# Performance work log

Hardware: AMD Instinct MI355X
Metric: run time of the kernel (lower is better)

The kernel has to match this reference:

```python
import jax, jax.numpy as jnp
import numpy as np

N_NODES = 50000
N_EDGES = 800000
D_IN = 128
D_OUT = 128
N_GRAPHS = 64
NEG_SLOPE = 0.01  # torch F.leaky_relu default


def gcn_conv(x, W, b, src, dst, n_nodes):
    """PyG GCNConv: linear, add self-loops, symmetric norm, scatter-add, bias."""
    h = x @ W  # [N, D_OUT]
    # degree including self-loop (edge_weight = 1)
    deg = jnp.zeros((n_nodes,), x.dtype).at[dst].add(1.0) + 1.0
    dinv = jax.lax.rsqrt(deg)
    norm = dinv[src] * dinv[dst]           # [E]
    agg = jnp.zeros_like(h).at[dst].add(h[src] * norm[:, None])
    # self-loop contribution: dinv[i]*dinv[i]*h[i] = h[i]/deg[i]
    return agg + h * (1.0 / deg)[:, None] + b


def gcn_branch(x, edge_index, Ws, bs):
    src, dst = edge_index[0], edge_index[1]
    n = x.shape[0]
    for W, b in zip(Ws, bs):
        x = gcn_conv(x, W, b, src, dst, n)
        x = jax.nn.leaky_relu(x, NEG_SLOPE)
        # dropout is identity in eval mode
    return x


def mean_pool(x, batch, num_graphs):
    s = jax.ops.segment_sum(x, batch, num_segments=num_graphs)
    cnt = jax.ops.segment_sum(jnp.ones((x.shape[0],), x.dtype), batch, num_segments=num_graphs)
    return s / jnp.maximum(cnt, 1.0)[:, None]


def setup_inputs() -> dict:
    key = jax.random.key(0)
    ks = jax.random.split(key, 20)
    inp = {
        'x1': jax.random.normal(ks[0], (N_NODES, D_IN), jnp.float32),
        'edge_index1': jax.random.randint(ks[1], (2, N_EDGES), 0, N_NODES, jnp.int64 if jax.config.jax_enable_x64 else jnp.int32),
        'batch1': jnp.sort(jax.random.randint(ks[2], (N_NODES,), 0, N_GRAPHS)),
        'x2': jax.random.normal(ks[3], (N_NODES, D_IN), jnp.float32),
        'edge_index2': jax.random.randint(ks[4], (2, N_EDGES), 0, N_NODES, jnp.int64 if jax.config.jax_enable_x64 else jnp.int32),
        'batch2': jnp.sort(jax.random.randint(ks[5], (N_NODES,), 0, N_GRAPHS)),
    }
    s = 1.0 / np.sqrt(D_IN)
    inp['W1_0'] = jax.random.uniform(ks[6], (D_IN, D_OUT), jnp.float32, -s, s)
    inp['b1_0'] = jnp.zeros((D_OUT,), jnp.float32)
    inp['W1_1'] = jax.random.uniform(ks[7], (D_OUT, D_OUT), jnp.float32, -s, s)
    inp['b1_1'] = jnp.zeros((D_OUT,), jnp.float32)
    inp['W2_0'] = jax.random.uniform(ks[8], (D_IN, D_OUT), jnp.float32, -s, s)
    inp['b2_0'] = jnp.zeros((D_OUT,), jnp.float32)
    inp['W2_1'] = jax.random.uniform(ks[9], (D_OUT, D_OUT), jnp.float32, -s, s)
    inp['b2_1'] = jnp.zeros((D_OUT,), jnp.float32)
    s2 = 1.0 / np.sqrt(2 * D_OUT)
    inp['lin1_W'] = jax.random.uniform(ks[10], (2 * D_OUT, D_OUT), jnp.float32, -s2, s2)
    inp['lin1_b'] = jax.random.uniform(ks[11], (D_OUT,), jnp.float32, -s2, s2)
    s3 = 1.0 / np.sqrt(D_OUT)
    inp['lin2_W'] = jax.random.uniform(ks[12], (D_OUT, 1), jnp.float32, -s3, s3)
    inp['lin2_b'] = jax.random.uniform(ks[13], (1,), jnp.float32, -s3, s3)
    return inp


def reference(x1, edge_index1, batch1, x2, edge_index2, batch2,
              W1_0, b1_0, W1_1, b1_1, W2_0, b2_0, W2_1, b2_1,
              lin1_W, lin1_b, lin2_W, lin2_b):
    h1 = gcn_branch(x1, edge_index1, [W1_0, W1_1], [b1_0, b1_1])
    h1 = mean_pool(h1, batch1, N_GRAPHS)
    h2 = gcn_branch(x2, edge_index2, [W2_0, W2_1], [b2_0, b2_1])
    h2 = mean_pool(h2, batch2, N_GRAPHS)
    h = jnp.concatenate([h1, h2], axis=-1)  # [G, 256]
    h = jax.nn.relu(h @ lin1_W + lin1_b)
    return h @ lin2_W + lin2_b  # [G, 1]
```

## Files before the change

### kernel.cpp

```cpp
#include <hip/hip_runtime.h>
#include <hip/hip_fp16.h>

#define N_NODES 50000
#define N_EDGES 800000
#define D 128
#define N_GRAPHS 64
#define NEG_SLOPE 0.01f
#define ELLW 32
#define OVF_CAP 8192

#define BUCKETS 196
#define NPAD (BUCKETS * 256)
#define EPB 2048
#define BCAP 5120
#define XS 136
#define NR (N_NODES + 16)
#define EMPTY_IDX 50000
#define EMPTY_FILL 0xC350C350u

typedef _Float16 half8 __attribute__((ext_vector_type(8)));
typedef _Float16 half4 __attribute__((ext_vector_type(4)));
typedef float f32x4 __attribute__((ext_vector_type(4)));
typedef float f32x2 __attribute__((ext_vector_type(2)));

__device__ __forceinline__ int lower_bound_i(const int* __restrict__ arr, int n, int key) {
    int lo = 0, hi = n;
    while (lo < hi) {
        int mid = (lo + hi) >> 1;
        if (arr[mid] < key) lo = mid + 1; else hi = mid;
    }
    return lo;
}

__global__ __launch_bounds__(256) void k_prep(const float* __restrict__ Wa, const float* __restrict__ Wb,
                                              const float* __restrict__ Wc, const float* __restrict__ Wd,
                                              const int* __restrict__ batch1, const int* __restrict__ batch2,
                                              __half* __restrict__ WtH, int* __restrict__ gcnt,
                                              float* __restrict__ pp, int* __restrict__ cntg,
                                              unsigned char* __restrict__ H8a, unsigned char* __restrict__ H8b) {
    const float* Ws[4] = {Wa, Wb, Wc, Wd};
    const float* W = Ws[blockIdx.x];
    __half* o = WtH + (size_t)blockIdx.x * 16384;
    int t = threadIdx.x;
    for (int r = 0; r < 64; r++) {
        int e = r * 256 + t;
        int k = e >> 7, n = e & 127;
        o[n * 128 + k] = __float2half(W[k * 128 + n]);
    }
#pragma unroll
    for (int i = 0; i < 16; i++) pp[blockIdx.x * 4096 + i * 256 + t] = 0.0f;
    {
        unsigned char* z = (blockIdx.x < 2 ? H8a : H8b) + (size_t)(blockIdx.x & 1) * NR * 128 + (size_t)N_NODES * 128;
        if (t < 32) ((unsigned int*)z)[t] = 0u;
    }
    if (blockIdx.x == 0) {
        for (int i = t; i < 2 * BUCKETS + 8; i += 256) gcnt[i] = 0;
    }
    if (blockIdx.x == 1) {
        if (t < 64)
            cntg[t] = lower_bound_i(batch1, N_NODES, t + 1) - lower_bound_i(batch1, N_NODES, t);
        else if (t < 128)
            cntg[t] = lower_bound_i(batch2, N_NODES, (t - 64) + 1) - lower_bound_i(batch2, N_NODES, t - 64);
    }
}

__global__ __launch_bounds__(256) void k_part(const int* __restrict__ ei1, const int* __restrict__ ei2,
                                              int* __restrict__ gcnt, int2* __restrict__ bucketed) {
    const int br = blockIdx.x & 1;
    const int blk = blockIdx.x >> 1;
    const int* __restrict__ src = (br ? ei2 : ei1);
    const int* __restrict__ dst = src + N_EDGES;
    int* __restrict__ gc = gcnt + br * BUCKETS;
    int2* __restrict__ bk = bucketed + (size_t)br * BUCKETS * BCAP;

    __shared__ int bcnt[BUCKETS];
    __shared__ int bofs[BUCKETS];
    __shared__ int gbase[BUCKETS];
    __shared__ int sc[BUCKETS];
    __shared__ int stot;
    __shared__ int2 stage[EPB];
    const int tid = threadIdx.x;
    const int base = blk * EPB;
    for (int b = tid; b < BUCKETS; b += 256) bcnt[b] = 0;
    __syncthreads();
    int d_[8], s_[8], p_[8];
#pragma unroll
    for (int k = 0; k < 8; k++) {
        int i = base + k * 256 + tid;
        bool v = i < N_EDGES;
        d_[k] = v ? dst[i] : -1;
        s_[k] = v ? src[i] : 0;
        p_[k] = 0;
        if (v) p_[k] = atomicAdd(&bcnt[d_[k] >> 8], 1);
    }
    __syncthreads();
    if (tid < BUCKETS) sc[tid] = bcnt[tid];
    __syncthreads();
    for (int off = 1; off < BUCKETS; off <<= 1) {
        int v = (tid < BUCKETS && tid >= off) ? sc[tid - off] : 0;
        __syncthreads();
        if (tid < BUCKETS) sc[tid] += v;
        __syncthreads();
    }
    if (tid < BUCKETS) {
        bofs[tid] = sc[tid] - bcnt[tid];
        gbase[tid] = atomicAdd(&gc[tid], bcnt[tid]);
    }
    if (tid == BUCKETS - 1) stot = sc[tid];
    __syncthreads();
#pragma unroll
    for (int k = 0; k < 8; k++) {
        if (d_[k] >= 0) stage[bofs[d_[k] >> 8] + p_[k]] = make_int2(d_[k], s_[k]);
    }
    __syncthreads();
    int total = stot;
    for (int i = tid; i < total; i += 256) {
        int2 e = stage[i];
        int b = e.x >> 8;
        int dest = gbase[b] + (i - bofs[b]);
        if (dest < BCAP) bk[(size_t)b * BCAP + dest] = e;
    }
}

__global__ __launch_bounds__(256) void k_build(const int* __restrict__ gcnt, const int2* __restrict__ bucketed,
                                               int* __restrict__ cnti, unsigned short* __restrict__ ell,
                                               int2* __restrict__ ovf, int* __restrict__ ocnt) {
    const int br = blockIdx.x & 1;
    const int b = blockIdx.x >> 1;
    const int* __restrict__ gc = gcnt + br * BUCKETS;
    const int2* __restrict__ bk = bucketed + (size_t)br * BUCKETS * BCAP;
    int* __restrict__ ci = cnti + br * NPAD;
    unsigned short* __restrict__ el = ell + (size_t)br * NPAD * ELLW;
    int2* __restrict__ ov = ovf + (size_t)br * OVF_CAP;
    int* __restrict__ oc = ocnt + br;

    __shared__ unsigned short lell[256 * ELLW];
    __shared__ int lcnt[256];
    const int tid = threadIdx.x;
    lcnt[tid] = 0;
#pragma unroll
    for (int i = 0; i < 4; i++) ((uint4*)lell)[tid + 256 * i] = make_uint4(EMPTY_FILL, EMPTY_FILL, EMPTY_FILL, EMPTY_FILL);
    __syncthreads();
    int nb = min(gc[b], BCAP);
    const int2* __restrict__ bp = bk + (size_t)b * BCAP;
    for (int i = tid; i < nb; i += 256) {
        int2 e = bp[i];
        int dl = e.x & 255;
        int p = atomicAdd(&lcnt[dl], 1);
        if (p < ELLW) {
            lell[dl * ELLW + p] = (unsigned short)e.y;
        } else {
            int o = atomicAdd(oc, 1);
            if (o < OVF_CAP) ov[o] = e;
        }
    }
    __syncthreads();
    ci[b * 256 + tid] = lcnt[tid];
    uint4* eg = (uint4*)(el + (size_t)b * 256 * ELLW);
    const uint4* elc = (const uint4*)lell;
    for (int i = tid; i < 256 * ELLW * 2 / 16; i += 256) eg[i] = elc[i];
}

template <bool FP16IN>
__global__ __launch_bounds__(256) void k_gemm(const void* __restrict__ xin1, const void* __restrict__ xin2,
                                              const __half* __restrict__ WtHall, int layer,
                                              const int* __restrict__ cnti, unsigned char* __restrict__ H8) {
    const int br = blockIdx.y;
    const void* __restrict__ xin = (br ? xin2 : xin1);
    const __half* __restrict__ WtH = WtHall + (size_t)(br * 2 + layer) * 16384;
    const int* __restrict__ cnt = cnti + br * NPAD;
    unsigned char* __restrict__ h = H8 + (size_t)br * NR * 128;

    __shared__ _Float16 Xl[64 * XS];
    __shared__ _Float16 Wt[128 * XS];
    const int tid = threadIdx.x;
    const int w = tid >> 6, lane = tid & 63;
    const int quad = lane >> 4, l16 = lane & 15;
    const int row0 = blockIdx.x * 64;

#pragma unroll
    for (int i = 0; i < 8; i++) {
        int i2 = tid + 256 * i;
        int r = i2 >> 4, cg = i2 & 15;
        *(uint4*)&Wt[r * XS + cg * 8] = ((const uint4*)WtH)[i2];
    }
    if (FP16IN) {
        const __half* x = (const __half*)xin;
#pragma unroll
        for (int i = 0; i < 4; i++) {
            int i2 = tid + 256 * i;
            int r = i2 >> 4, cg = i2 & 15;
            uint4 v = make_uint4(0, 0, 0, 0);
            if (row0 + r < N_NODES) v = ((const uint4*)(x + (size_t)(row0 + r) * D))[cg];
            *(uint4*)&Xl[r * XS + cg * 8] = v;
        }
    } else {
        const float* x = (const float*)xin;
#pragma unroll
        for (int i = 0; i < 8; i++) {
            int i2 = tid + 256 * i;
            int r = i2 >> 5, f4 = i2 & 31;
            float4 v = make_float4(0.f, 0.f, 0.f, 0.f);
            if (row0 + r < N_NODES) v = *(const float4*)((const float*)x + (size_t)(row0 + r) * D + f4 * 4);
            half4 hv;
            hv[0] = (_Float16)v.x; hv[1] = (_Float16)v.y; hv[2] = (_Float16)v.z; hv[3] = (_Float16)v.w;
            *(half4*)&Xl[r * XS + f4 * 4] = hv;
        }
    }
    __syncthreads();

    half8 a[4];
#pragma unroll
    for (int kb = 0; kb < 4; kb++)
        a[kb] = *(const half8*)&Xl[(w * 16 + l16) * XS + kb * 32 + quad * 8];

    const int rbase = row0 + w * 16 + quad * 4;
    float di[4];
#pragma unroll
    for (int reg = 0; reg < 4; reg++) {
        int r = rbase + reg;
        di[reg] = (r < N_NODES) ? rsqrtf((float)cnt[r] + 1.0f) : 0.0f;
    }

    float accs[8][4];
#pragma unroll
    for (int ct = 0; ct < 8; ct++) {
        f32x4 acc = {0.f, 0.f, 0.f, 0.f};
#pragma unroll
        for (int kb = 0; kb < 4; kb++) {
            half8 b = *(const half8*)&Wt[(ct * 16 + l16) * XS + kb * 32 + quad * 8];
            acc = __builtin_amdgcn_mfma_f32_16x16x32_f16(a[kb], b, acc, 0, 0, 0);
        }
#pragma unroll
        for (int reg = 0; reg < 4; reg++) accs[ct][reg] = acc[reg] * di[reg];
    }

    __syncthreads();
    unsigned char* S = (unsigned char*)Xl;
#pragma unroll
    for (int ct = 0; ct < 8; ct++)
#pragma unroll
        for (int reg = 0; reg < 4; reg++) {
            int p = __builtin_amdgcn_cvt_pk_fp8_f32(accs[ct][reg], accs[ct][reg], 0, false);
            S[(w * 16 + quad * 4 + reg) * 128 + ct * 16 + l16] = (unsigned char)p;
        }
    __syncthreads();
#pragma unroll
    for (int i = 0; i < 2; i++) {
        int idx = tid + 256 * i;
        int r = idx >> 3, cg = idx & 7;
        if (row0 + r < N_NODES)
            ((uint4*)(h + (size_t)(row0 + r) * 128))[cg] = ((const uint4*)S)[idx];
    }
}

#define AGG_ISSUE(buf, g) do {                                                             \
    unsigned int iw0 = *(const unsigned int*)&sidx[hw][(g) * 8 + 0];                       \
    unsigned int iw1 = *(const unsigned int*)&sidx[hw][(g) * 8 + 2];                       \
    unsigned int iw2 = *(const unsigned int*)&sidx[hw][(g) * 8 + 4];                       \
    unsigned int iw3 = *(const unsigned int*)&sidx[hw][(g) * 8 + 6];                       \
    buf[0] = *(const unsigned int*)(H8 + (size_t)(iw0 & 0xffffu) * 128 + l32 * 4);         \
    buf[1] = *(const unsigned int*)(H8 + (size_t)(iw0 >> 16) * 128 + l32 * 4);             \
    buf[2] = *(const unsigned int*)(H8 + (size_t)(iw1 & 0xffffu) * 128 + l32 * 4);         \
    buf[3] = *(const unsigned int*)(H8 + (size_t)(iw1 >> 16) * 128 + l32 * 4);             \
    buf[4] = *(const unsigned int*)(H8 + (size_t)(iw2 & 0xffffu) * 128 + l32 * 4);         \
    buf[5] = *(const unsigned int*)(H8 + (size_t)(iw2 >> 16) * 128 + l32 * 4);             \
    buf[6] = *(const unsigned int*)(H8 + (size_t)(iw3 & 0xffffu) * 128 + l32 * 4);         \
    buf[7] = *(const unsigned int*)(H8 + (size_t)(iw3 >> 16) * 128 + l32 * 4);             \
} while (0)

#define AGG_CONSUME(buf) do {                                                              \
    _Pragma("unroll")                                                                      \
    for (int i_ = 0; i_ < 8; i_++) {                                                       \
        f32x2 lo = __builtin_amdgcn_cvt_pk_f32_fp8((int)buf[i_], false);                   \
        f32x2 hi = __builtin_amdgcn_cvt_pk_f32_fp8((int)buf[i_], true);                    \
        accv[i_ & 3].x += lo[0];                                                           \
        accv[i_ & 3].y += lo[1];                                                           \
        accv[i_ & 3].z += hi[0];                                                           \
        accv[i_ & 3].w += hi[1];                                                           \
    }                                                                                      \
} while (0)

#define AGG_CORE()                                                                         \
    float4 accv[4];                                                                        \
    {                                                                                      \
        f32x2 lo = __builtin_amdgcn_cvt_pk_f32_fp8((int)dself, false);                     \
        f32x2 hi = __builtin_amdgcn_cvt_pk_f32_fp8((int)dself, true);                      \
        accv[0] = make_float4(lo[0], lo[1], hi[0], hi[1]);                                 \
    }                                                                                      \
    accv[1] = make_float4(0.f, 0.f, 0.f, 0.f); accv[2] = accv[1]; accv[3] = accv[1];       \
    unsigned int bA_[8], bB_[8], bC_[8], bD_[8];                                           \
    AGG_ISSUE(bA_, 0);                                                                     \
    if (jmax > 8)  { AGG_ISSUE(bB_, 1); }                                                  \
    if (jmax > 16) { AGG_ISSUE(bC_, 2); }                                                  \
    if (jmax > 24) { AGG_ISSUE(bD_, 3); }                                                  \
    AGG_CONSUME(bA_);                                                                      \
    if (jmax > 8)  { AGG_CONSUME(bB_); }                                                   \
    if (jmax > 16) { AGG_CONSUME(bC_); }                                                   \
    if (jmax > 24) { AGG_CONSUME(bD_); }

__global__ __launch_bounds__(256) void k_agg(const int* __restrict__ cnti, const unsigned short* __restrict__ ell,
                                             const int2* __restrict__ ovf, const int* __restrict__ ocnt,
                                             const unsigned char* __restrict__ H8all, const float* __restrict__ bias1,
                                             const float* __restrict__ bias2, __half* __restrict__ ACT) {
    const int tid = threadIdx.x;
    const int l32 = tid & 31;
    const int hw = tid >> 5;
    const int br = blockIdx.x & 1;
    const int blk = blockIdx.x >> 1;
    const int node = blk * 8 + hw;

    const int* __restrict__ cnt = cnti + br * NPAD;
    const unsigned short* __restrict__ el = ell + (size_t)br * NPAD * ELLW;
    const int2* __restrict__ ov = ovf + (size_t)br * OVF_CAP;
    const unsigned char* __restrict__ H8 = H8all + (size_t)br * NR * 128;
    const float* __restrict__ bias = (br ? bias2 : bias1);
    __half* __restrict__ out = ACT + (size_t)br * N_NODES * D;

    __shared__ unsigned short sidx[8][ELLW];
    if (tid < 32) ((uint4*)sidx)[tid] = ((const uint4*)(el + (size_t)blk * 8 * ELLW))[tid];

    int n = cnt[node];
    int nc = min(n, ELLW);
    int ncO = __shfl(nc, (tid & 63) ^ 32, 64);
    int jmax = max(nc, ncO);
    unsigned int dself = *(const unsigned int*)(H8 + (size_t)node * 128 + l32 * 4);
    __syncthreads();

    AGG_CORE();

    if (n > ELLW) {
        int oc = min(ocnt[br], OVF_CAP);
        for (int o = 0; o < oc; o++) {
            int2 p = ov[o];
            if (p.x == node) {
                unsigned int dw = *(const unsigned int*)(H8 + (size_t)p.y * 128 + l32 * 4);
                f32x2 lo = __builtin_amdgcn_cvt_pk_f32_fp8((int)dw, false);
                f32x2 hi = __builtin_amdgcn_cvt_pk_f32_fp8((int)dw, true);
                accv[0].x += lo[0]; accv[0].y += lo[1]; accv[0].z += hi[0]; accv[0].w += hi[1];
            }
        }
    }
    float sx = (accv[0].x + accv[1].x) + (accv[2].x + accv[3].x);
    float sy = (accv[0].y + accv[1].y) + (accv[2].y + accv[3].y);
    float sz = (accv[0].z + accv[1].z) + (accv[2].z + accv[3].z);
    float sw = (accv[0].w + accv[1].w) + (accv[2].w + accv[3].w);
    float dv = rsqrtf((float)n + 1.0f);
    float4 b = ((const float4*)bias)[l32];
    float vx = sx * dv + b.x;
    float vy = sy * dv + b.y;
    float vz = sz * dv + b.z;
    float vw = sw * dv + b.w;
    vx = vx > 0.0f ? vx : NEG_SLOPE * vx;
    vy = vy > 0.0f ? vy : NEG_SLOPE * vy;
    vz = vz > 0.0f ? vz : NEG_SLOPE * vz;
    vw = vw > 0.0f ? vw : NEG_SLOPE * vw;
    union { __half2 h2[2]; uint2 u; } up;
    up.h2[0] = __floats2half2_rn(vx, vy);
    up.h2[1] = __floats2half2_rn(vz, vw);
    *(uint2*)(out + (size_t)node * 128 + l32 * 4) = up.u;
}

__global__ __launch_bounds__(256) void k_aggpool(const int* __restrict__ cnti, const unsigned short* __restrict__ ell,
                                                 const int2* __restrict__ ovf, const int* __restrict__ ocnt,
                                                 const unsigned char* __restrict__ H8all,
                                                 const float* __restrict__ bias1, const float* __restrict__ bias2,
                                                 const int* __restrict__ batch1, const int* __restrict__ batch2,
                                                 float* __restrict__ ppall) {
    const int tid = threadIdx.x;
    const int l32 = tid & 31;
    const int hw = tid >> 5;
    const int br = blockIdx.x & 1;
    const int blk = blockIdx.x >> 1;
    const int node = blk * 8 + hw;

    const int* __restrict__ cnt = cnti + br * NPAD;
    const unsigned short* __restrict__ el = ell + (size_t)br * NPAD * ELLW;
    const int2* __restrict__ ov = ovf + (size_t)br * OVF_CAP;
    const unsigned char* __restrict__ H8 = H8all + (size_t)br * NR * 128;
    const float* __restrict__ bias = (br ? bias2 : bias1);
    const int* __restrict__ batch = (br ? batch2 : batch1);
    float* __restrict__ pp = ppall + (size_t)br * N_GRAPHS * D;

    __shared__ unsigned short sidx[8][ELLW];
    if (tid < 32) ((uint4*)sidx)[tid] = ((const uint4*)(el + (size_t)blk * 8 * ELLW))[tid];

    int n = cnt[node];
    int nc = min(n, ELLW);
    int ncO = __shfl(nc, (tid & 63) ^ 32, 64);
    int jmax = max(nc, ncO);
    unsigned int dself = *(const unsigned int*)(H8 + (size_t)node * 128 + l32 * 4);
    __syncthreads();

    AGG_CORE();

    if (n > ELLW) {
        int oc = min(ocnt[br], OVF_CAP);
        for (int o = 0; o < oc; o++) {
            int2 p = ov[o];
            if (p.x == node) {
                unsigned int dw = *(const unsigned int*)(H8 + (size_t)p.y * 128 + l32 * 4);
                f32x2 lo = __builtin_amdgcn_cvt_pk_f32_fp8((int)dw, false);
                f32x2 hi = __builtin_amdgcn_cvt_pk_f32_fp8((int)dw, true);
                accv[0].x += lo[0]; accv[0].y += lo[1]; accv[0].z += hi[0]; accv[0].w += hi[1];
            }
        }
    }
    float sx = (accv[0].x + accv[1].x) + (accv[2].x + accv[3].x);
    float sy = (accv[0].y + accv[1].y) + (accv[2].y + accv[3].y);
    float sz = (accv[0].z + accv[1].z) + (accv[2].z + accv[3].z);
    float sw = (accv[0].w + accv[1].w) + (accv[2].w + accv[3].w);
    float dv = rsqrtf((float)n + 1.0f);
    float4 b = ((const float4*)bias)[l32];
    float vx = sx * dv + b.x;
    float vy = sy * dv + b.y;
    float vz = sz * dv + b.z;
    float vw = sw * dv + b.w;
    vx = vx > 0.0f ? vx : NEG_SLOPE * vx;
    vy = vy > 0.0f ? vy : NEG_SLOPE * vy;
    vz = vz > 0.0f ? vz : NEG_SLOPE * vz;
    vw = vw > 0.0f ? vw : NEG_SLOPE * vw;
    __half2 q0 = __floats2half2_rn(vx, vy);
    __half2 q1 = __floats2half2_rn(vz, vw);
    float2 f0 = __half22float2(q0);
    float2 f1 = __half22float2(q1);

    __shared__ float sacc[8][128];
    __shared__ int sg[8];
    *(float4*)&sacc[hw][l32 * 4] = make_float4(f0.x, f0.y, f1.x, f1.y);
    if (l32 == 0) sg[hw] = batch[node];
    __syncthreads();
    if (tid < 128) {
        float s = sacc[0][tid];
        int g = sg[0];
        for (int r2 = 1; r2 < 8; r2++) {
            if (sg[r2] == g) {
                s += sacc[r2][tid];
            } else {
                atomicAdd(&pp[(size_t)g * D + tid], s);
                s = sacc[r2][tid];
                g = sg[r2];
            }
        }
        atomicAdd(&pp[(size_t)g * D + tid], s);
    }
}

__global__ __launch_bounds__(128) void k_mlp(const float* __restrict__ pp, const int* __restrict__ cntg,
                                             const float* __restrict__ lin1W, const float* __restrict__ lin1b,
                                             const float* __restrict__ lin2W, const float* __restrict__ lin2b,
                                             float* __restrict__ out) {
    int g = blockIdx.x;
    int c = threadIdx.x;
    __shared__ float cat[2 * D];
    cat[c] = pp[(size_t)g * D + c] / fmaxf((float)cntg[g], 1.0f);
    cat[c + D] = pp[(size_t)(N_GRAPHS + g) * D + c] / fmaxf((float)cntg[64 + g], 1.0f);
    __syncthreads();
    float acc = lin1b[c];
#pragma unroll 8
    for (int k = 0; k < 2 * D; k++) acc += cat[k] * lin1W[k * D + c];
    acc = fmaxf(acc, 0.0f);
    float v = acc * lin2W[c];
#pragma unroll
    for (int off = 32; off > 0; off >>= 1) v += __shfl_down(v, off, 64);
    __shared__ float wsum[2];
    if ((c & 63) == 0) wsum[c >> 6] = v;
    __syncthreads();
    if (c == 0) out[g] = wsum[0] + wsum[1] + lin2b[0];
}

extern "C" void kernel_launch(void* const* d_in, const int* in_sizes, int n_in,
                              void* d_out, int out_size, void* d_ws, size_t ws_size,
                              hipStream_t stream) {
    const float* x1 = (const float*)d_in[0];
    const int*   ei1 = (const int*)d_in[1];
    const int*   batch1 = (const int*)d_in[2];
    const float* x2 = (const float*)d_in[3];
    const int*   ei2 = (const int*)d_in[4];
    const int*   batch2 = (const int*)d_in[5];
    const float* W1_0 = (const float*)d_in[6];
    const float* b1_0 = (const float*)d_in[7];
    const float* W1_1 = (const float*)d_in[8];
    const float* b1_1 = (const float*)d_in[9];
    const float* W2_0 = (const float*)d_in[10];
    const float* b2_0 = (const float*)d_in[11];
    const float* W2_1 = (const float*)d_in[12];
    const float* b2_1 = (const float*)d_in[13];
    const float* lin1W = (const float*)d_in[14];
    const float* lin1b = (const float*)d_in[15];
    const float* lin2W = (const float*)d_in[16];
    const float* lin2b = (const float*)d_in[17];
    float* out = (float*)d_out;

    __half* WtH = (__half*)d_ws;
    __half* ACT = WtH + 65536;
    unsigned char* H8a = (unsigned char*)(ACT + 2 * (size_t)N_NODES * D);
    unsigned char* H8b = H8a + 2 * (size_t)NR * 128;
    unsigned short* ell = (unsigned short*)(H8b + 2 * (size_t)NR * 128);
    int2*   bucketed = (int2*)(ell + 2 * (size_t)NPAD * ELLW);
    int*    cnti = (int*)(bucketed + 2 * (size_t)BUCKETS * BCAP);
    int*    gcnt = cnti + 2 * NPAD;
    int*    ocnt = gcnt + 2 * BUCKETS;
    int*    cntg = ocnt + 8;
    int2*   ovf  = (int2*)(cntg + 128);
    float*  pp   = (float*)(ovf + 2 * (size_t)OVF_CAP);

    dim3 b256(256);
    int partBlocks = (N_EDGES + EPB - 1) / EPB;
    int gemmBlocks = (N_NODES + 63) / 64;
    int aggBlocks  = N_NODES / 8;

    k_prep<<<4, b256, 0, stream>>>(W1_0, W1_1, W2_0, W2_1, batch1, batch2, WtH, gcnt, pp, cntg, H8a, H8b);

    k_part  <<<partBlocks * 2, b256, 0, stream>>>(ei1, ei2, gcnt, bucketed);
    k_build <<<BUCKETS * 2,    b256, 0, stream>>>(gcnt, bucketed, cnti, ell, ovf, ocnt);

    k_gemm<false><<<dim3(gemmBlocks, 2), b256, 0, stream>>>(x1, x2, WtH, 0, cnti, H8a);
    k_agg        <<<aggBlocks * 2,       b256, 0, stream>>>(cnti, ell, ovf, ocnt, H8a, b1_0, b2_0, ACT);
    k_gemm<true> <<<dim3(gemmBlocks, 2), b256, 0, stream>>>(ACT, ACT + (size_t)N_NODES * D, WtH, 1, cnti, H8b);
    k_aggpool    <<<aggBlocks * 2,       b256, 0, stream>>>(cnti, ell, ovf, ocnt, H8b, b1_1, b2_1, batch1, batch2, pp);

    k_mlp<<<N_GRAPHS, dim3(128), 0, stream>>>(pp, cntg, lin1W, lin1b, lin2W, lin2b, out);
}
```

Measured before the change: 283.6 us.

## Split aggregation feature dim into halves with 16 lanes per node

The aggregation kernels now give each node 16 lanes covering half of the 128 feature columns, with the two column halves handled by separate grid blocks, so 16 nodes share a block. Each node then branches on its own neighbor count instead of the max over two nodes sharing a wavefront. The goal is to cut wasted gather work caused by degree divergence inside a wave. The cost is that each node's ELL indices and count are read twice (once per half), each gather is a narrower 64-byte row segment, and the pooling stage issues twice as many atomics on narrower rows.

```diff
diff --git a/kernel.cpp b/kernel.cpp
--- a/kernel.cpp
+++ b/kernel.cpp
@@ -17,6 +17,7 @@
 #define NR (N_NODES + 16)
 #define EMPTY_IDX 50000
 #define EMPTY_FILL 0xC350C350u
+#define AGG_BLKS (N_NODES / 16)
 
 typedef _Float16 half8 __attribute__((ext_vector_type(8)));
 typedef _Float16 half4 __attribute__((ext_vector_type(4)));
@@ -255,18 +256,18 @@
 }
 
 #define AGG_ISSUE(buf, g) do {                                                             \
-    unsigned int iw0 = *(const unsigned int*)&sidx[hw][(g) * 8 + 0];                       \
-    unsigned int iw1 = *(const unsigned int*)&sidx[hw][(g) * 8 + 2];                       \
-    unsigned int iw2 = *(const unsigned int*)&sidx[hw][(g) * 8 + 4];                       \
-    unsigned int iw3 = *(const unsigned int*)&sidx[hw][(g) * 8 + 6];                       \
-    buf[0] = *(const unsigned int*)(H8 + (size_t)(iw0 & 0xffffu) * 128 + l32 * 4);         \
-    buf[1] = *(const unsigned int*)(H8 + (size_t)(iw0 >> 16) * 128 + l32 * 4);             \
-    buf[2] = *(const unsigned int*)(H8 + (size_t)(iw1 & 0xffffu) * 128 + l32 * 4);         \
-    buf[3] = *(const unsigned int*)(H8 + (size_t)(iw1 >> 16) * 128 + l32 * 4);             \
-    buf[4] = *(const unsigned int*)(H8 + (size_t)(iw2 & 0xffffu) * 128 + l32 * 4);         \
-    buf[5] = *(const unsigned int*)(H8 + (size_t)(iw2 >> 16) * 128 + l32 * 4);             \
-    buf[6] = *(const unsigned int*)(H8 + (size_t)(iw3 & 0xffffu) * 128 + l32 * 4);         \
-    buf[7] = *(const unsigned int*)(H8 + (size_t)(iw3 >> 16) * 128 + l32 * 4);             \
+    unsigned int iw0 = *(const unsigned int*)&sidx[nq][(g) * 8 + 0];                       \
+    unsigned int iw1 = *(const unsigned int*)&sidx[nq][(g) * 8 + 2];                       \
+    unsigned int iw2 = *(const unsigned int*)&sidx[nq][(g) * 8 + 4];                       \
+    unsigned int iw3 = *(const unsigned int*)&sidx[nq][(g) * 8 + 6];                       \
+    buf[0] = *(const unsigned int*)(H8 + (size_t)(iw0 & 0xffffu) * 128 + hofs + l16 * 4);  \
+    buf[1] = *(const unsigned int*)(H8 + (size_t)(iw0 >> 16) * 128 + hofs + l16 * 4);      \
+    buf[2] = *(const unsigned int*)(H8 + (size_t)(iw1 & 0xffffu) * 128 + hofs + l16 * 4);  \
+    buf[3] = *(const unsigned int*)(H8 + (size_t)(iw1 >> 16) * 128 + hofs + l16 * 4);      \
+    buf[4] = *(const unsigned int*)(H8 + (size_t)(iw2 & 0xffffu) * 128 + hofs + l16 * 4);  \
+    buf[5] = *(const unsigned int*)(H8 + (size_t)(iw2 >> 16) * 128 + hofs + l16 * 4);      \
+    buf[6] = *(const unsigned int*)(H8 + (size_t)(iw3 & 0xffffu) * 128 + hofs + l16 * 4);  \
+    buf[7] = *(const unsigned int*)(H8 + (size_t)(iw3 >> 16) * 128 + hofs + l16 * 4);      \
 } while (0)
 
 #define AGG_CONSUME(buf) do {                                                              \
@@ -291,24 +292,27 @@
     accv[1] = make_float4(0.f, 0.f, 0.f, 0.f); accv[2] = accv[1]; accv[3] = accv[1];       \
     unsigned int bA_[8], bB_[8], bC_[8], bD_[8];                                           \
     AGG_ISSUE(bA_, 0);                                                                     \
-    if (jmax > 8)  { AGG_ISSUE(bB_, 1); }                                                  \
-    if (jmax > 16) { AGG_ISSUE(bC_, 2); }                                                  \
-    if (jmax > 24) { AGG_ISSUE(bD_, 3); }                                                  \
+    if (nc > 8)  { AGG_ISSUE(bB_, 1); }                                                    \
+    if (nc > 16) { AGG_ISSUE(bC_, 2); }                                                    \
+    if (nc > 24) { AGG_ISSUE(bD_, 3); }                                                    \
     AGG_CONSUME(bA_);                                                                      \
-    if (jmax > 8)  { AGG_CONSUME(bB_); }                                                   \
-    if (jmax > 16) { AGG_CONSUME(bC_); }                                                   \
-    if (jmax > 24) { AGG_CONSUME(bD_); }
+    if (nc > 8)  { AGG_CONSUME(bB_); }                                                     \
+    if (nc > 16) { AGG_CONSUME(bC_); }                                                     \
+    if (nc > 24) { AGG_CONSUME(bD_); }
 
 __global__ __launch_bounds__(256) void k_agg(const int* __restrict__ cnti, const unsigned short* __restrict__ ell,
                                              const int2* __restrict__ ovf, const int* __restrict__ ocnt,
                                              const unsigned char* __restrict__ H8all, const float* __restrict__ bias1,
                                              const float* __restrict__ bias2, __half* __restrict__ ACT) {
     const int tid = threadIdx.x;
-    const int l32 = tid & 31;
-    const int hw = tid >> 5;
+    const int l16 = tid & 15;
+    const int nq = tid >> 4;
     const int br = blockIdx.x & 1;
-    const int blk = blockIdx.x >> 1;
-    const int node = blk * 8 + hw;
+    const int rest = blockIdx.x >> 1;
+    const int half = rest >= AGG_BLKS ? 1 : 0;
+    const int blk = rest - half * AGG_BLKS;
+    const int node = blk * 16 + nq;
+    const int hofs = half * 64;
 
     const int* __restrict__ cnt = cnti + br * NPAD;
     const unsigned short* __restrict__ el = ell + (size_t)br * NPAD * ELLW;
@@ -317,14 +321,12 @@
     const float* __restrict__ bias = (br ? bias2 : bias1);
     __half* __restrict__ out = ACT + (size_t)br * N_NODES * D;
 
-    __shared__ unsigned short sidx[8][ELLW];
-    if (tid < 32) ((uint4*)sidx)[tid] = ((const uint4*)(el + (size_t)blk * 8 * ELLW))[tid];
+    __shared__ unsigned short sidx[16][ELLW];
+    if (tid < 64) ((uint4*)sidx)[tid] = ((const uint4*)(el + (size_t)blk * 16 * ELLW))[tid];
 
     int n = cnt[node];
     int nc = min(n, ELLW);
-    int ncO = __shfl(nc, (tid & 63) ^ 32, 64);
-    int jmax = max(nc, ncO);
-    unsigned int dself = *(const unsigned int*)(H8 + (size_t)node * 128 + l32 * 4);
+    unsigned int dself = *(const unsigned int*)(H8 + (size_t)node * 128 + hofs + l16 * 4);
     __syncthreads();
 
     AGG_CORE();
@@ -334,7 +336,7 @@
         for (int o = 0; o < oc; o++) {
             int2 p = ov[o];
             if (p.x == node) {
-                unsigned int dw = *(const unsigned int*)(H8 + (size_t)p.y * 128 + l32 * 4);
+                unsigned int dw = *(const unsigned int*)(H8 + (size_t)p.y * 128 + hofs + l16 * 4);
                 f32x2 lo = __builtin_amdgcn_cvt_pk_f32_fp8((int)dw, false);
                 f32x2 hi = __builtin_amdgcn_cvt_pk_f32_fp8((int)dw, true);
                 accv[0].x += lo[0]; accv[0].y += lo[1]; accv[0].z += hi[0]; accv[0].w += hi[1];
@@ -346,7 +348,7 @@
     float sz = (accv[0].z + accv[1].z) + (accv[2].z + accv[3].z);
     float sw = (accv[0].w + accv[1].w) + (accv[2].w + accv[3].w);
     float dv = rsqrtf((float)n + 1.0f);
-    float4 b = ((const float4*)bias)[l32];
+    float4 b = ((const float4*)bias)[half * 16 + l16];
     float vx = sx * dv + b.x;
     float vy = sy * dv + b.y;
     float vz = sz * dv + b.z;
@@ -358,7 +360,7 @@
     union { __half2 h2[2]; uint2 u; } up;
     up.h2[0] = __floats2half2_rn(vx, vy);
     up.h2[1] = __floats2half2_rn(vz, vw);
-    *(uint2*)(out + (size_t)node * 128 + l32 * 4) = up.u;
+    *(uint2*)(out + (size_t)node * 128 + half * 64 + l16 * 4) = up.u;
 }
 
 __global__ __launch_bounds__(256) void k_aggpool(const int* __restrict__ cnti, const unsigned short* __restrict__ ell,
@@ -368,11 +370,14 @@
                                                  const int* __restrict__ batch1, const int* __restrict__ batch2,
                                                  float* __restrict__ ppall) {
     const int tid = threadIdx.x;
-    const int l32 = tid & 31;
-    const int hw = tid >> 5;
+    const int l16 = tid & 15;
+    const int nq = tid >> 4;
     const int br = blockIdx.x & 1;
-    const int blk = blockIdx.x >> 1;
-    const int node = blk * 8 + hw;
+    const int rest = blockIdx.x >> 1;
+    const int half = rest >= AGG_BLKS ? 1 : 0;
+    const int blk = rest - half * AGG_BLKS;
+    const int node = blk * 16 + nq;
+    const int hofs = half * 64;
 
     const int* __restrict__ cnt = cnti + br * NPAD;
     const unsigned short* __restrict__ el = ell + (size_t)br * NPAD * ELLW;
@@ -382,14 +387,12 @@
     const int* __restrict__ batch = (br ? batch2 : batch1);
     float* __restrict__ pp = ppall + (size_t)br * N_GRAPHS * D;
 
-    __shared__ unsigned short sidx[8][ELLW];
-    if (tid < 32) ((uint4*)sidx)[tid] = ((const uint4*)(el + (size_t)blk * 8 * ELLW))[tid];
+    __shared__ unsigned short sidx[16][ELLW];
+    if (tid < 64) ((uint4*)sidx)[tid] = ((const uint4*)(el + (size_t)blk * 16 * ELLW))[tid];
 
     int n = cnt[node];
     int nc = min(n, ELLW);
-    int ncO = __shfl(nc, (tid & 63) ^ 32, 64);
-    int jmax = max(nc, ncO);
-    unsigned int dself = *(const unsigned int*)(H8 + (size_t)node * 128 + l32 * 4);
+    unsigned int dself = *(const unsigned int*)(H8 + (size_t)node * 128 + hofs + l16 * 4);
     __syncthreads();
 
     AGG_CORE();
@@ -399,7 +402,7 @@
         for (int o = 0; o < oc; o++) {
             int2 p = ov[o];
             if (p.x == node) {
-                unsigned int dw = *(const unsigned int*)(H8 + (size_t)p.y * 128 + l32 * 4);
+                unsigned int dw = *(const unsigned int*)(H8 + (size_t)p.y * 128 + hofs + l16 * 4);
                 f32x2 lo = __builtin_amdgcn_cvt_pk_f32_fp8((int)dw, false);
                 f32x2 hi = __builtin_amdgcn_cvt_pk_f32_fp8((int)dw, true);
                 accv[0].x += lo[0]; accv[0].y += lo[1]; accv[0].z += hi[0]; accv[0].w += hi[1];
@@ -411,7 +414,7 @@
     float sz = (accv[0].z + accv[1].z) + (accv[2].z + accv[3].z);
     float sw = (accv[0].w + accv[1].w) + (accv[2].w + accv[3].w);
     float dv = rsqrtf((float)n + 1.0f);
-    float4 b = ((const float4*)bias)[l32];
+    float4 b = ((const float4*)bias)[half * 16 + l16];
     float vx = sx * dv + b.x;
     float vy = sy * dv + b.y;
     float vz = sz * dv + b.z;
@@ -425,24 +428,24 @@
     float2 f0 = __half22float2(q0);
     float2 f1 = __half22float2(q1);
 
-    __shared__ float sacc[8][128];
-    __shared__ int sg[8];
-    *(float4*)&sacc[hw][l32 * 4] = make_float4(f0.x, f0.y, f1.x, f1.y);
-    if (l32 == 0) sg[hw] = batch[node];
-    __syncthreads();
-    if (tid < 128) {
+    __shared__ float sacc[16][64];
+    __shared__ int sg[16];
+    *(float4*)&sacc[nq][l16 * 4] = make_float4(f0.x, f0.y, f1.x, f1.y);
+    if (l16 == 0) sg[nq] = batch[node];
+    __syncthreads();
+    if (tid < 64) {
         float s = sacc[0][tid];
         int g = sg[0];
-        for (int r2 = 1; r2 < 8; r2++) {
+        for (int r2 = 1; r2 < 16; r2++) {
             if (sg[r2] == g) {
                 s += sacc[r2][tid];
             } else {
-                atomicAdd(&pp[(size_t)g * D + tid], s);
+                atomicAdd(&pp[(size_t)g * D + half * 64 + tid], s);
                 s = sacc[r2][tid];
                 g = sg[r2];
             }
         }
-        atomicAdd(&pp[(size_t)g * D + tid], s);
+        atomicAdd(&pp[(size_t)g * D + half * 64 + tid], s);
     }
 }
 
@@ -508,7 +511,7 @@
     dim3 b256(256);
     int partBlocks = (N_EDGES + EPB - 1) / EPB;
     int gemmBlocks = (N_NODES + 63) / 64;
-    int aggBlocks  = N_NODES / 8;
+    int aggGrid    = AGG_BLKS * 4;
 
     k_prep<<<4, b256, 0, stream>>>(W1_0, W1_1, W2_0, W2_1, batch1, batch2, WtH, gcnt, pp, cntg, H8a, H8b);
 
@@ -516,9 +519,9 @@
     k_build <<<BUCKETS * 2,    b256, 0, stream>>>(gcnt, bucketed, cnti, ell, ovf, ocnt);
 
     k_gemm<false><<<dim3(gemmBlocks, 2), b256, 0, stream>>>(x1, x2, WtH, 0, cnti, H8a);
-    k_agg        <<<aggBlocks * 2,       b256, 0, stream>>>(cnti, ell, ovf, ocnt, H8a, b1_0, b2_0, ACT);
+    k_agg        <<<aggGrid,             b256, 0, stream>>>(cnti, ell, ovf, ocnt, H8a, b1_0, b2_0, ACT);
     k_gemm<true> <<<dim3(gemmBlocks, 2), b256, 0, stream>>>(ACT, ACT + (size_t)N_NODES * D, WtH, 1, cnti, H8b);
-    k_aggpool    <<<aggBlocks * 2,       b256, 0, stream>>>(cnti, ell, ovf, ocnt, H8b, b1_1, b2_1, batch1, batch2, pp);
+    k_aggpool    <<<aggGrid,             b256, 0, stream>>>(cnti, ell, ovf, ocnt, H8b, b1_1, b2_1, batch1, batch2, pp);
 
     k_mlp<<<N_GRAPHS, dim3(128), 0, stream>>>(pp, cntg, lin1W, lin1b, lin2W, lin2b, out);
 }
```

Measured after the change: 280.6 us (median of 2 runs). Within noise of the previous version (-1.0%).
